# Kernel tuning notes

Hardware: AMD Instinct MI355X
Metric: run time of the kernel (lower is better)

Reference implementation:

```python
import math
import jax, jax.numpy as jnp
import numpy as np

B, S, D, H, V = 8, 1024, 512, 8, 32000
HD = D // H


def _position_embedding(seq_len, d_model):
    pos = jnp.arange(seq_len, dtype=jnp.float32)[:, None]                 # [S,1]
    div = jnp.exp(jnp.arange(0, d_model, 2, dtype=jnp.float32) * (-math.log(10000.0) / d_model))  # [D/2]
    ang = pos * div                                                        # [S,D/2]
    # interleave sin (even cols) / cos (odd cols)
    return jnp.stack([jnp.sin(ang), jnp.cos(ang)], axis=-1).reshape(seq_len, d_model)


def _min_max_normalize(w):
    lo = jnp.min(w, axis=-1, keepdims=True)
    hi = jnp.max(w, axis=-1, keepdims=True)
    return (w - lo) / (hi - lo)


def _converable_mask(h, Wc, bc):
    bs, seq = h.shape[0], h.shape[1]
    half = seq // 2
    shift = math.ceil(seq / 2)
    width = jnp.einsum('bsd,od->bso', h, Wc)[..., 0] + bc[0]               # [B,S]
    width = _min_max_normalize(width)[..., None]                           # [B,S,1]
    origin = jnp.concatenate([jnp.linspace(1.0, 0.0, half),
                              jnp.linspace(0.0, 1.0, seq - half)])         # [S]
    origin_mask = 1.0 - jax.nn.sigmoid((origin[None, None, :] - width) * 100.0)  # [B,S,S]
    idx = (jnp.arange(seq - 1, -1, -1)[:, None] + jnp.arange(seq)[None, :]) % seq  # [S,S]
    idx = jnp.roll(idx, shift, axis=0)
    # torch.roll of a [1,S] row along dim 0 is a no-op
    cmp = idx >= jnp.arange(seq)[None, :]                                  # [S,S] bool
    move = jnp.concatenate([cmp[:shift], ~cmp[shift:]], axis=0)            # [S,S]
    gathered = jnp.take_along_axis(origin_mask, idx[None, :, :], axis=2)   # [B,S,S]
    return gathered * move.astype(origin_mask.dtype)


def setup_inputs():
    key = jax.random.key(0)
    ks = jax.random.split(key, 9)
    s_emb = 1.0
    s_hd = 1.0 / math.sqrt(HD)
    s_d = 1.0 / math.sqrt(D)
    return {
        'x':   jax.random.randint(ks[0], (B, S), 0, V),
        'emb': jax.random.normal(ks[1], (V, D), dtype=jnp.float32) * s_emb,
        'Wq':  jax.random.normal(ks[2], (HD, HD), dtype=jnp.float32) * s_hd,
        'Wk':  jax.random.normal(ks[3], (HD, HD), dtype=jnp.float32) * s_hd,
        'Wv':  jax.random.normal(ks[4], (HD, HD), dtype=jnp.float32) * s_hd,
        'Wo':  jax.random.normal(ks[5], (D, D), dtype=jnp.float32) * s_d,
        'bo':  jnp.zeros((D,), dtype=jnp.float32),
        'Wc':  jax.random.normal(ks[6], (1, D), dtype=jnp.float32) * s_d,
        'bc':  jnp.zeros((1,), dtype=jnp.float32),
    }


def reference(x, emb, Wq, Wk, Wv, Wo, bo, Wc, bc):
    h = emb[x] + _position_embedding(S, D)[None]                           # [B,S,D]
    mask = _converable_mask(h, Wc, bc)                                     # [B,S,S]
    hh = h.reshape(B, S, H, HD)
    q = jnp.einsum('bshd,od->bsho', hh, Wq)
    k = jnp.einsum('bshd,od->bsho', hh, Wk)
    v = jnp.einsum('bshd,od->bsho', hh, Wv)
    energy = jnp.einsum('bqhd,bkhd->bhqk', q, k)                           # [B,H,S,S]
    # mask [B,S,S] broadcasts as [1,B,S,S]; valid because B == H (as in original)
    energy = energy * mask
    attn = jax.nn.softmax(energy / math.sqrt(D), axis=3)
    out = jnp.einsum('bhqk,bkhd->bqhd', attn, v).reshape(B, S, D)
    out = out @ Wo.T + bo
    return (out, mask)
```

## Files before the change

### kernel.cpp

```cpp
#include <hip/hip_runtime.h>
#include <hip/hip_bf16.h>
#include <math.h>

#define Bn 8
#define Sn 1024
#define Dn 512
#define Hn 8
#define HDn 64

typedef __bf16 bf16x8 __attribute__((ext_vector_type(8)));
typedef __bf16 bf16x4 __attribute__((ext_vector_type(4)));
typedef __bf16 bf16x2 __attribute__((ext_vector_type(2)));
typedef float  f32x4  __attribute__((ext_vector_type(4)));
typedef float  f32x16 __attribute__((ext_vector_type(16)));
typedef unsigned int u32x4 __attribute__((ext_vector_type(4)));

__device__ __forceinline__ unsigned enc_f(float v) {
    unsigned u = __float_as_uint(v);
    return (u & 0x80000000u) ? ~u : (u | 0x80000000u);
}
__device__ __forceinline__ float dec_f(unsigned k) {
    unsigned u = (k & 0x80000000u) ? (k ^ 0x80000000u) : ~k;
    return __uint_as_float(u);
}

__global__ __launch_bounds__(256) void k_fused(
        const int* __restrict__ x, const float* __restrict__ emb,
        const float* __restrict__ Wc, const float* __restrict__ bc,
        const float* __restrict__ Wq, const float* __restrict__ Wk,
        const float* __restrict__ Wv,
        float* __restrict__ width, unsigned* __restrict__ lohi,
        __bf16* __restrict__ q, __bf16* __restrict__ k, __bf16* __restrict__ vt) {
    __shared__ __align__(16) __bf16 Xs[64][72];
    __shared__ __align__(16) __bf16 WqS[64][72];
    __shared__ __align__(16) __bf16 WkS[64][72];
    __shared__ __align__(16) __bf16 WvS[64][72];
    __shared__ float wtok[8];
    int t = threadIdx.x;
    int bs0 = blockIdx.x * 8;
    int m0 = blockIdx.x * 64;
    int w = t >> 6, lane = t & 63, quad = lane >> 4, li = lane & 15;

    {
        int token = t >> 5, l32 = t & 31;
        int bs = bs0 + token;
        int s = bs & (Sn - 1);
        int tok = x[bs];
        float wpart = 0.f;
        int row = token * 8 + ((l32 * 16) >> 6);
        #pragma unroll
        for (int j = 0; j < 4; ++j) {
            int d0 = l32 * 16 + j * 4;
            float4 ev = *(const float4*)&emb[(size_t)tok * Dn + d0];
            float4 wc = *(const float4*)&Wc[d0];
            float hv[4];
            #pragma unroll
            for (int i = 0; i < 4; ++i) {
                int d = d0 + i;
                float f = __expf((float)(d & ~1) * (-9.210340371976184f / 512.0f));
                float ang = (float)s * f;
                float pe = (d & 1) ? __cosf(ang) : __sinf(ang);
                hv[i] = (&ev.x)[i] + pe;
                wpart += hv[i] * (&wc.x)[i];
            }
            *(bf16x4*)&Xs[row][d0 & 63] =
                (bf16x4){(__bf16)hv[0], (__bf16)hv[1], (__bf16)hv[2], (__bf16)hv[3]};
        }
        #pragma unroll
        for (int off = 1; off < 32; off <<= 1) wpart += __shfl_xor(wpart, off);
        if (l32 == 0) { float wv = wpart + bc[0]; width[bs] = wv; wtok[token] = wv; }
    }
    #pragma unroll
    for (int it = 0; it < 4; ++it) {
        int e = (it * 256 + t) * 4; int r = e >> 6, c = e & 63;
        float4 qv = *(const float4*)&Wq[e];
        *(bf16x4*)&WqS[r][c] = (bf16x4){(__bf16)qv.x, (__bf16)qv.y, (__bf16)qv.z, (__bf16)qv.w};
        float4 kv = *(const float4*)&Wk[e];
        *(bf16x4*)&WkS[r][c] = (bf16x4){(__bf16)kv.x, (__bf16)kv.y, (__bf16)kv.z, (__bf16)kv.w};
        float4 vv = *(const float4*)&Wv[e];
        *(bf16x4*)&WvS[r][c] = (bf16x4){(__bf16)vv.x, (__bf16)vv.y, (__bf16)vv.z, (__bf16)vv.w};
    }
    __syncthreads();

    if (t == 0) {
        float mn = wtok[0], mx = wtok[0];
        #pragma unroll
        for (int i = 1; i < 8; ++i) { mn = fminf(mn, wtok[i]); mx = fmaxf(mx, wtok[i]); }
        int b = bs0 >> 10;
        atomicMin(&lohi[b], enc_f(mn));
        atomicMin(&lohi[8 + b], ~enc_f(mx));
    }

    bf16x8 A0 = *(const bf16x8*)&Xs[w * 16 + li][quad * 8];
    bf16x8 A1 = *(const bf16x8*)&Xs[w * 16 + li][32 + quad * 8];
    f32x4 aq[4], ak[4], av[4];
    #pragma unroll
    for (int n = 0; n < 4; ++n) {
        aq[n] = (f32x4){0.f,0.f,0.f,0.f}; ak[n] = aq[n]; av[n] = aq[n];
        bf16x8 Bq0 = *(const bf16x8*)&WqS[n * 16 + li][quad * 8];
        bf16x8 Bq1 = *(const bf16x8*)&WqS[n * 16 + li][32 + quad * 8];
        aq[n] = __builtin_amdgcn_mfma_f32_16x16x32_bf16(A0, Bq0, aq[n], 0, 0, 0);
        aq[n] = __builtin_amdgcn_mfma_f32_16x16x32_bf16(A1, Bq1, aq[n], 0, 0, 0);
        bf16x8 Bk0 = *(const bf16x8*)&WkS[n * 16 + li][quad * 8];
        bf16x8 Bk1 = *(const bf16x8*)&WkS[n * 16 + li][32 + quad * 8];
        ak[n] = __builtin_amdgcn_mfma_f32_16x16x32_bf16(A0, Bk0, ak[n], 0, 0, 0);
        ak[n] = __builtin_amdgcn_mfma_f32_16x16x32_bf16(A1, Bk1, ak[n], 0, 0, 0);
        bf16x8 Bv0 = *(const bf16x8*)&WvS[n * 16 + li][quad * 8];
        bf16x8 Bv1 = *(const bf16x8*)&WvS[n * 16 + li][32 + quad * 8];
        av[n] = __builtin_amdgcn_mfma_f32_16x16x32_bf16(A0, Bv0, av[n], 0, 0, 0);
        av[n] = __builtin_amdgcn_mfma_f32_16x16x32_bf16(A1, Bv1, av[n], 0, 0, 0);
    }

    #pragma unroll
    for (int n = 0; n < 4; ++n)
        #pragma unroll
        for (int r = 0; r < 4; ++r) {
            int Rg = m0 + w * 16 + quad * 4 + r;
            int bsI = Rg >> 3, head = Rg & 7;
            int b = bsI >> 10, s = bsI & (Sn - 1);
            size_t oidx = (((size_t)(b * Hn + head)) * Sn + s) * HDn + n * 16 + li;
            q[oidx] = (__bf16)aq[n][r];
            k[oidx] = (__bf16)ak[n][r];
        }

    __bf16 (*Vs)[72] = WqS;
    __syncthreads();
    #pragma unroll
    for (int n = 0; n < 4; ++n)
        #pragma unroll
        for (int r = 0; r < 4; ++r)
            Vs[w * 16 + quad * 4 + r][n * 16 + li] = (__bf16)av[n][r];
    __syncthreads();
    int bs0i = m0 >> 3;
    int b = bs0i >> 10, s0l = bs0i & (Sn - 1);
    #pragma unroll
    for (int i = 0; i < 2; ++i) {
        int p = t + 256 * i;
        int head = p >> 6, o = p & 63;
        __bf16 tmp[8];
        #pragma unroll
        for (int j = 0; j < 8; ++j) tmp[j] = Vs[j * 8 + head][o];
        *(bf16x8*)&vt[(((size_t)(b * Hn + head)) * HDn + o) * Sn + s0l] = *(bf16x8*)tmp;
    }
}

__global__ void k_mask(const float* __restrict__ width, const unsigned* __restrict__ lohi,
                       float* __restrict__ mask_out, __bf16* __restrict__ maskb) {
    const float SCALE = 0.04419417382415922f;
    int bs = blockIdx.x;
    int b = bs >> 10;
    int s = bs & (Sn - 1);
    float lo = dec_f(lohi[b]);
    float hi = dec_f(~lohi[8 + b]);
    float wn = (width[bs] - lo) / (hi - lo);
    for (int t = threadIdx.x; t < Sn; t += 256) {
        int it = (t - s + 1535) & (Sn - 1);
        float origin = (it < 512) ? (1.0f - (float)it * (1.0f / 511.0f))
                                  : ((float)(it - 512) * (1.0f / 511.0f));
        float z = (origin - wn) * 100.0f;
        float om;
        if (z >= 0.0f) { float e = __expf(-z); om = e / (1.0f + e); }
        else           { float e = __expf(z);  om = 1.0f / (1.0f + e); }
        bool cmpv = (it >= t);
        bool mv = (s < 512) ? cmpv : !cmpv;
        float val = mv ? om : 0.0f;
        mask_out[(size_t)bs * Sn + t] = val;
        maskb[(size_t)bs * Sn + t] = (__bf16)(val * SCALE);
    }
}

__global__ __launch_bounds__(256, 2) void k_attn(
        const __bf16* __restrict__ q, const __bf16* __restrict__ k,
        const __bf16* __restrict__ vt, const __bf16* __restrict__ maskb,
        __bf16* __restrict__ ao) {
    __shared__ __align__(16) __bf16 Ks[2][64][72];
    __shared__ __align__(16) __bf16 Vt[2][64][72];
    int blk = blockIdx.x;
    int hh = blk & 7;
    int qt = (blk >> 3) & 7;
    int b  = blk >> 6;
    int bh = b * Hn + hh;
    int q0 = qt * 128;
    int t = threadIdx.x;
    int w = t >> 6, lane = t & 63, hi5 = lane >> 5, l31 = lane & 31;

    const __bf16* qbase  = q  + ((size_t)bh * Sn + q0 + w * 32) * HDn;
    const __bf16* kbase  = k  + (size_t)bh * Sn * HDn;
    const __bf16* vtbase = vt + (size_t)bh * HDn * Sn;
    const __bf16* mq = maskb + ((size_t)hh * Sn + q0 + w * 32 + l31) * Sn;

    bf16x8 Qf[4];
    #pragma unroll
    for (int c = 0; c < 4; ++c)
        Qf[c] = *(const bf16x8*)&qbase[(size_t)l31 * HDn + c * 16 + hi5 * 8];

    int sr0 = t >> 3, sc0 = (t & 7) * 8;
    bf16x8 pk0, pk1, pv0, pv1;
    pk0 = *(const bf16x8*)&kbase[(size_t)sr0 * HDn + sc0];
    pk1 = *(const bf16x8*)&kbase[(size_t)(sr0 + 32) * HDn + sc0];
    pv0 = *(const bf16x8*)&vtbase[(size_t)sr0 * Sn + sc0];
    pv1 = *(const bf16x8*)&vtbase[(size_t)(sr0 + 32) * Sn + sc0];
    *(bf16x8*)&Ks[0][sr0][sc0] = pk0;
    *(bf16x8*)&Ks[0][sr0 + 32][sc0] = pk1;
    *(bf16x8*)&Vt[0][sr0][sc0] = pv0;
    *(bf16x8*)&Vt[0][sr0 + 32][sc0] = pv1;
    __syncthreads();

    f32x16 OT[2];
    OT[0] = (f32x16){0.f,0.f,0.f,0.f,0.f,0.f,0.f,0.f,0.f,0.f,0.f,0.f,0.f,0.f,0.f,0.f};
    OT[1] = OT[0];
    float rs = 0.f;

    for (int ti = 0; ti < 16; ++ti) {
        int cur = ti & 1;

        bf16x4 mk[2][4];
        #pragma unroll
        for (int kg = 0; kg < 2; ++kg)
            #pragma unroll
            for (int g = 0; g < 4; ++g)
                mk[kg][g] = *(const bf16x4*)&mq[ti * 64 + kg * 32 + g * 8 + hi5 * 4];

        if (ti < 15) {
            int k0n = (ti + 1) * 64;
            pk0 = *(const bf16x8*)&kbase[(size_t)(k0n + sr0) * HDn + sc0];
            pk1 = *(const bf16x8*)&kbase[(size_t)(k0n + sr0 + 32) * HDn + sc0];
            pv0 = *(const bf16x8*)&vtbase[(size_t)sr0 * Sn + k0n + sc0];
            pv1 = *(const bf16x8*)&vtbase[(size_t)(sr0 + 32) * Sn + k0n + sc0];
        }

        f32x16 St[2];
        St[0] = (f32x16){0.f,0.f,0.f,0.f,0.f,0.f,0.f,0.f,0.f,0.f,0.f,0.f,0.f,0.f,0.f,0.f};
        St[1] = St[0];
        __builtin_amdgcn_s_setprio(1);
        #pragma unroll
        for (int c = 0; c < 4; ++c) {
            bf16x8 K0 = *(const bf16x8*)&Ks[cur][l31][c * 16 + hi5 * 8];
            St[0] = __builtin_amdgcn_mfma_f32_32x32x16_bf16(K0, Qf[c], St[0], 0, 0, 0);
            bf16x8 K1 = *(const bf16x8*)&Ks[cur][32 + l31][c * 16 + hi5 * 8];
            St[1] = __builtin_amdgcn_mfma_f32_32x32x16_bf16(K1, Qf[c], St[1], 0, 0, 0);
        }
        __builtin_amdgcn_s_setprio(0);

        unsigned pkd[2][4][2];
        #pragma unroll
        for (int kg = 0; kg < 2; ++kg) {
            #pragma unroll
            for (int g = 0; g < 4; ++g) {
                float p0 = __expf(St[kg][4 * g + 0] * (float)mk[kg][g][0]);
                float p1 = __expf(St[kg][4 * g + 1] * (float)mk[kg][g][1]);
                float p2 = __expf(St[kg][4 * g + 2] * (float)mk[kg][g][2]);
                float p3 = __expf(St[kg][4 * g + 3] * (float)mk[kg][g][3]);
                rs += (p0 + p1) + (p2 + p3);
                bf16x2 plo = { (__bf16)p0, (__bf16)p1 };
                bf16x2 phi = { (__bf16)p2, (__bf16)p3 };
                pkd[kg][g][0] = __builtin_bit_cast(unsigned, plo);
                pkd[kg][g][1] = __builtin_bit_cast(unsigned, phi);
            }
        }

        __builtin_amdgcn_s_setprio(1);
        #pragma unroll
        for (int c = 0; c < 4; ++c) {
            const int kg = c >> 1, gA = 2 * (c & 1), gB = gA + 1;
            unsigned z0 = hi5 ? pkd[kg][gB][0] : pkd[kg][gA][0];
            unsigned z1 = hi5 ? pkd[kg][gB][1] : pkd[kg][gA][1];
            unsigned y0 = hi5 ? pkd[kg][gA][0] : pkd[kg][gB][0];
            unsigned y1 = hi5 ? pkd[kg][gA][1] : pkd[kg][gB][1];
            unsigned x0 = (unsigned)__shfl_xor((int)y0, 32);
            unsigned x1 = (unsigned)__shfl_xor((int)y1, 32);
            u32x4 du;
            du[0] = hi5 ? x0 : z0;
            du[1] = hi5 ? x1 : z1;
            du[2] = hi5 ? z0 : x0;
            du[3] = hi5 ? z1 : x1;
            bf16x8 Pf = __builtin_bit_cast(bf16x8, du);
            bf16x8 V0 = *(const bf16x8*)&Vt[cur][l31][c * 16 + hi5 * 8];
            OT[0] = __builtin_amdgcn_mfma_f32_32x32x16_bf16(V0, Pf, OT[0], 0, 0, 0);
            bf16x8 V1 = *(const bf16x8*)&Vt[cur][32 + l31][c * 16 + hi5 * 8];
            OT[1] = __builtin_amdgcn_mfma_f32_32x32x16_bf16(V1, Pf, OT[1], 0, 0, 0);
        }
        __builtin_amdgcn_s_setprio(0);

        if (ti < 15) {
            *(bf16x8*)&Ks[cur ^ 1][sr0][sc0] = pk0;
            *(bf16x8*)&Ks[cur ^ 1][sr0 + 32][sc0] = pk1;
            *(bf16x8*)&Vt[cur ^ 1][sr0][sc0] = pv0;
            *(bf16x8*)&Vt[cur ^ 1][sr0 + 32][sc0] = pv1;
            __syncthreads();
        }
    }

    rs += __shfl_xor(rs, 32);
    float inv = __fdividef(1.0f, rs);

    size_t orow = ((size_t)b * Sn + q0 + w * 32 + l31) * Dn + hh * HDn;
    #pragma unroll
    for (int og = 0; og < 2; ++og)
        #pragma unroll
        for (int g2 = 0; g2 < 4; ++g2) {
            bf16x4 ov = { (__bf16)(OT[og][4 * g2 + 0] * inv),
                          (__bf16)(OT[og][4 * g2 + 1] * inv),
                          (__bf16)(OT[og][4 * g2 + 2] * inv),
                          (__bf16)(OT[og][4 * g2 + 3] * inv) };
            *(bf16x4*)&ao[orow + og * 32 + g2 * 8 + hi5 * 4] = ov;
        }
}

__global__ __launch_bounds__(256) void k_proj(
        const __bf16* __restrict__ ao, const float* __restrict__ Wo,
        const float* __restrict__ bo, float* __restrict__ out) {
    __shared__ __align__(16) __bf16 As[64][72];
    __shared__ __align__(16) __bf16 Bs[64][72];
    int bm = blockIdx.x >> 3;
    int bn = blockIdx.x & 7;
    int m0 = bm * 64, n0 = bn * 64;
    int t = threadIdx.x;
    int w = t >> 6, lane = t & 63, quad = lane >> 4, li = lane & 15;

    f32x4 O[4];
    #pragma unroll
    for (int n = 0; n < 4; ++n) O[n] = (f32x4){0.f, 0.f, 0.f, 0.f};

    for (int k0 = 0; k0 < Dn; k0 += 64) {
        if (k0) __syncthreads();
        #pragma unroll
        for (int it = 0; it < 2; ++it) {
            int e = (it * 256 + t) * 8; int r = e >> 6, c = e & 63;
            *(bf16x8*)&As[r][c] = *(const bf16x8*)&ao[(size_t)(m0 + r) * Dn + k0 + c];
        }
        #pragma unroll
        for (int it = 0; it < 4; ++it) {
            int e = (it * 256 + t) * 4; int r = e >> 6, c = e & 63;
            float4 wv = *(const float4*)&Wo[(size_t)(n0 + r) * Dn + k0 + c];
            *(bf16x4*)&Bs[r][c] = (bf16x4){(__bf16)wv.x, (__bf16)wv.y, (__bf16)wv.z, (__bf16)wv.w};
        }
        __syncthreads();

        bf16x8 A0 = *(const bf16x8*)&As[w * 16 + li][quad * 8];
        bf16x8 A1 = *(const bf16x8*)&As[w * 16 + li][32 + quad * 8];
        #pragma unroll
        for (int n = 0; n < 4; ++n) {
            bf16x8 B0 = *(const bf16x8*)&Bs[n * 16 + li][quad * 8];
            O[n] = __builtin_amdgcn_mfma_f32_16x16x32_bf16(A0, B0, O[n], 0, 0, 0);
            bf16x8 B1 = *(const bf16x8*)&Bs[n * 16 + li][32 + quad * 8];
            O[n] = __builtin_amdgcn_mfma_f32_16x16x32_bf16(A1, B1, O[n], 0, 0, 0);
        }
    }

    #pragma unroll
    for (int n = 0; n < 4; ++n) {
        float bias = bo[n0 + n * 16 + li];
        #pragma unroll
        for (int r = 0; r < 4; ++r)
            out[(size_t)(m0 + w * 16 + quad * 4 + r) * Dn + n0 + n * 16 + li] = O[n][r] + bias;
    }
}

extern "C" void kernel_launch(void* const* d_in, const int* in_sizes, int n_in,
                              void* d_out, int out_size, void* d_ws, size_t ws_size,
                              hipStream_t stream) {
    const int*   x   = (const int*)d_in[0];
    const float* emb = (const float*)d_in[1];
    const float* Wq  = (const float*)d_in[2];
    const float* Wk  = (const float*)d_in[3];
    const float* Wv  = (const float*)d_in[4];
    const float* Wo  = (const float*)d_in[5];
    const float* bo  = (const float*)d_in[6];
    const float* Wc  = (const float*)d_in[7];
    const float* bc  = (const float*)d_in[8];

    float* ws      = (float*)d_ws;
    float* width   = ws;
    unsigned* lohi = (unsigned*)(width + Bn * Sn);
    __bf16* qb   = (__bf16*)(ws + Bn * Sn + 16);
    __bf16* kb   = qb + (size_t)Bn * Sn * Dn;
    __bf16* vtb  = kb + (size_t)Bn * Sn * Dn;
    __bf16* maskb = vtb + (size_t)Bn * Sn * Dn;
    __bf16* ao   = maskb + (size_t)Bn * Sn * Sn;

    float* out      = (float*)d_out;
    float* mask_out = out + (size_t)Bn * Sn * Dn;

    hipMemsetAsync(lohi, 0xFF, 16 * sizeof(unsigned), stream);
    k_fused<<<(Bn * Sn) / 8, 256, 0, stream>>>(x, emb, Wc, bc, Wq, Wk, Wv,
                                               width, lohi, qb, kb, vtb);
    k_mask<<<Bn * Sn, 256, 0, stream>>>(width, lohi, mask_out, maskb);
    k_attn<<<Bn * Hn * (Sn / 128), 256, 0, stream>>>(qb, kb, vtb, maskb, ao);
    k_proj<<<(Bn * Sn / 64) * (Dn / 64), 256, 0, stream>>>(ao, Wo, bo, out);
}
```

Measured before the change: 208.1 us.

## Drop bf16 mask copy, fold scale into Q, shrink attention blocks, coalesce stores

The separate bf16 scaled mask buffer is removed. Attention now reads the fp32 mask output directly, and the softmax scale is folded into Q in the projection kernel. Q/K stores in the fused kernel and the output stores in the projection kernel are staged through shared memory so each thread writes contiguous vectors. The attention kernel moves to 128-thread blocks covering 64 query rows each, doubling the grid. The trade is half the mask traffic and better store coalescing against twice the fp32 mask bytes read per attention tile and extra syncs.

```diff
diff --git a/kernel.cpp b/kernel.cpp
--- a/kernel.cpp
+++ b/kernel.cpp
@@ -111,26 +111,32 @@
         av[n] = __builtin_amdgcn_mfma_f32_16x16x32_bf16(A1, Bv1, av[n], 0, 0, 0);
     }
 
+    const float SCALE = 0.04419417382415922f;
+    __syncthreads();
     #pragma unroll
     for (int n = 0; n < 4; ++n)
         #pragma unroll
         for (int r = 0; r < 4; ++r) {
-            int Rg = m0 + w * 16 + quad * 4 + r;
-            int bsI = Rg >> 3, head = Rg & 7;
-            int b = bsI >> 10, s = bsI & (Sn - 1);
-            size_t oidx = (((size_t)(b * Hn + head)) * Sn + s) * HDn + n * 16 + li;
-            q[oidx] = (__bf16)aq[n][r];
-            k[oidx] = (__bf16)ak[n][r];
-        }
+            int row = w * 16 + quad * 4 + r, col = n * 16 + li;
+            WkS[row][col] = (__bf16)(aq[n][r] * SCALE);
+            WvS[row][col] = (__bf16)ak[n][r];
+            WqS[row][col] = (__bf16)av[n][r];
+        }
+    __syncthreads();
+
+    {
+        int row = t >> 2, part = (t & 3) * 16;
+        int Rg = m0 + row;
+        int bsI = Rg >> 3, head = Rg & 7;
+        int bq = bsI >> 10, sq = bsI & (Sn - 1);
+        size_t base = (((size_t)(bq * Hn + head)) * Sn + sq) * HDn + part;
+        *(bf16x8*)&q[base]     = *(bf16x8*)&WkS[row][part];
+        *(bf16x8*)&q[base + 8] = *(bf16x8*)&WkS[row][part + 8];
+        *(bf16x8*)&k[base]     = *(bf16x8*)&WvS[row][part];
+        *(bf16x8*)&k[base + 8] = *(bf16x8*)&WvS[row][part + 8];
+    }
 
     __bf16 (*Vs)[72] = WqS;
-    __syncthreads();
-    #pragma unroll
-    for (int n = 0; n < 4; ++n)
-        #pragma unroll
-        for (int r = 0; r < 4; ++r)
-            Vs[w * 16 + quad * 4 + r][n * 16 + li] = (__bf16)av[n][r];
-    __syncthreads();
     int bs0i = m0 >> 3;
     int b = bs0i >> 10, s0l = bs0i & (Sn - 1);
     #pragma unroll
@@ -145,8 +151,7 @@
 }
 
 __global__ void k_mask(const float* __restrict__ width, const unsigned* __restrict__ lohi,
-                       float* __restrict__ mask_out, __bf16* __restrict__ maskb) {
-    const float SCALE = 0.04419417382415922f;
+                       float* __restrict__ mask_out) {
     int bs = blockIdx.x;
     int b = bs >> 10;
     int s = bs & (Sn - 1);
@@ -163,47 +168,47 @@
         else           { float e = __expf(z);  om = 1.0f / (1.0f + e); }
         bool cmpv = (it >= t);
         bool mv = (s < 512) ? cmpv : !cmpv;
-        float val = mv ? om : 0.0f;
-        mask_out[(size_t)bs * Sn + t] = val;
-        maskb[(size_t)bs * Sn + t] = (__bf16)(val * SCALE);
-    }
-}
-
-__global__ __launch_bounds__(256, 2) void k_attn(
+        mask_out[(size_t)bs * Sn + t] = mv ? om : 0.0f;
+    }
+}
+
+__global__ __launch_bounds__(128, 2) void k_attn(
         const __bf16* __restrict__ q, const __bf16* __restrict__ k,
-        const __bf16* __restrict__ vt, const __bf16* __restrict__ maskb,
+        const __bf16* __restrict__ vt, const float* __restrict__ mask,
         __bf16* __restrict__ ao) {
     __shared__ __align__(16) __bf16 Ks[2][64][72];
     __shared__ __align__(16) __bf16 Vt[2][64][72];
     int blk = blockIdx.x;
     int hh = blk & 7;
-    int qt = (blk >> 3) & 7;
-    int b  = blk >> 6;
+    int qt = (blk >> 3) & 15;
+    int b  = blk >> 7;
     int bh = b * Hn + hh;
-    int q0 = qt * 128;
+    int q0 = qt * 64;
     int t = threadIdx.x;
     int w = t >> 6, lane = t & 63, hi5 = lane >> 5, l31 = lane & 31;
 
     const __bf16* qbase  = q  + ((size_t)bh * Sn + q0 + w * 32) * HDn;
     const __bf16* kbase  = k  + (size_t)bh * Sn * HDn;
     const __bf16* vtbase = vt + (size_t)bh * HDn * Sn;
-    const __bf16* mq = maskb + ((size_t)hh * Sn + q0 + w * 32 + l31) * Sn;
+    const float* mq = mask + ((size_t)hh * Sn + q0 + w * 32 + l31) * Sn;
 
     bf16x8 Qf[4];
     #pragma unroll
     for (int c = 0; c < 4; ++c)
         Qf[c] = *(const bf16x8*)&qbase[(size_t)l31 * HDn + c * 16 + hi5 * 8];
 
-    int sr0 = t >> 3, sc0 = (t & 7) * 8;
-    bf16x8 pk0, pk1, pv0, pv1;
-    pk0 = *(const bf16x8*)&kbase[(size_t)sr0 * HDn + sc0];
-    pk1 = *(const bf16x8*)&kbase[(size_t)(sr0 + 32) * HDn + sc0];
-    pv0 = *(const bf16x8*)&vtbase[(size_t)sr0 * Sn + sc0];
-    pv1 = *(const bf16x8*)&vtbase[(size_t)(sr0 + 32) * Sn + sc0];
-    *(bf16x8*)&Ks[0][sr0][sc0] = pk0;
-    *(bf16x8*)&Ks[0][sr0 + 32][sc0] = pk1;
-    *(bf16x8*)&Vt[0][sr0][sc0] = pv0;
-    *(bf16x8*)&Vt[0][sr0 + 32][sc0] = pv1;
+    int sr = t >> 3, sc = (t & 7) * 8;
+    bf16x8 pk[4], pv[4];
+    #pragma unroll
+    for (int j = 0; j < 4; ++j) {
+        pk[j] = *(const bf16x8*)&kbase[(size_t)(sr + j * 16) * HDn + sc];
+        pv[j] = *(const bf16x8*)&vtbase[(size_t)(sr + j * 16) * Sn + sc];
+    }
+    #pragma unroll
+    for (int j = 0; j < 4; ++j) {
+        *(bf16x8*)&Ks[0][sr + j * 16][sc] = pk[j];
+        *(bf16x8*)&Vt[0][sr + j * 16][sc] = pv[j];
+    }
     __syncthreads();
 
     f32x16 OT[2];
@@ -214,19 +219,20 @@
     for (int ti = 0; ti < 16; ++ti) {
         int cur = ti & 1;
 
-        bf16x4 mk[2][4];
+        float4 mk[2][4];
         #pragma unroll
         for (int kg = 0; kg < 2; ++kg)
             #pragma unroll
             for (int g = 0; g < 4; ++g)
-                mk[kg][g] = *(const bf16x4*)&mq[ti * 64 + kg * 32 + g * 8 + hi5 * 4];
+                mk[kg][g] = *(const float4*)&mq[ti * 64 + kg * 32 + g * 8 + hi5 * 4];
 
         if (ti < 15) {
             int k0n = (ti + 1) * 64;
-            pk0 = *(const bf16x8*)&kbase[(size_t)(k0n + sr0) * HDn + sc0];
-            pk1 = *(const bf16x8*)&kbase[(size_t)(k0n + sr0 + 32) * HDn + sc0];
-            pv0 = *(const bf16x8*)&vtbase[(size_t)sr0 * Sn + k0n + sc0];
-            pv1 = *(const bf16x8*)&vtbase[(size_t)(sr0 + 32) * Sn + k0n + sc0];
+            #pragma unroll
+            for (int j = 0; j < 4; ++j) {
+                pk[j] = *(const bf16x8*)&kbase[(size_t)(k0n + sr + j * 16) * HDn + sc];
+                pv[j] = *(const bf16x8*)&vtbase[(size_t)(sr + j * 16) * Sn + k0n + sc];
+            }
         }
 
         f32x16 St[2];
@@ -247,10 +253,10 @@
         for (int kg = 0; kg < 2; ++kg) {
             #pragma unroll
             for (int g = 0; g < 4; ++g) {
-                float p0 = __expf(St[kg][4 * g + 0] * (float)mk[kg][g][0]);
-                float p1 = __expf(St[kg][4 * g + 1] * (float)mk[kg][g][1]);
-                float p2 = __expf(St[kg][4 * g + 2] * (float)mk[kg][g][2]);
-                float p3 = __expf(St[kg][4 * g + 3] * (float)mk[kg][g][3]);
+                float p0 = __expf(St[kg][4 * g + 0] * mk[kg][g].x);
+                float p1 = __expf(St[kg][4 * g + 1] * mk[kg][g].y);
+                float p2 = __expf(St[kg][4 * g + 2] * mk[kg][g].z);
+                float p3 = __expf(St[kg][4 * g + 3] * mk[kg][g].w);
                 rs += (p0 + p1) + (p2 + p3);
                 bf16x2 plo = { (__bf16)p0, (__bf16)p1 };
                 bf16x2 phi = { (__bf16)p2, (__bf16)p3 };
@@ -283,10 +289,11 @@
         __builtin_amdgcn_s_setprio(0);
 
         if (ti < 15) {
-            *(bf16x8*)&Ks[cur ^ 1][sr0][sc0] = pk0;
-            *(bf16x8*)&Ks[cur ^ 1][sr0 + 32][sc0] = pk1;
-            *(bf16x8*)&Vt[cur ^ 1][sr0][sc0] = pv0;
-            *(bf16x8*)&Vt[cur ^ 1][sr0 + 32][sc0] = pv1;
+            #pragma unroll
+            for (int j = 0; j < 4; ++j) {
+                *(bf16x8*)&Ks[cur ^ 1][sr + j * 16][sc] = pk[j];
+                *(bf16x8*)&Vt[cur ^ 1][sr + j * 16][sc] = pv[j];
+            }
             __syncthreads();
         }
     }
@@ -312,6 +319,7 @@
         const float* __restrict__ bo, float* __restrict__ out) {
     __shared__ __align__(16) __bf16 As[64][72];
     __shared__ __align__(16) __bf16 Bs[64][72];
+    __shared__ __align__(16) float  Os[64][68];
     int bm = blockIdx.x >> 3;
     int bn = blockIdx.x & 7;
     int m0 = bm * 64, n0 = bn * 64;
@@ -353,7 +361,15 @@
         float bias = bo[n0 + n * 16 + li];
         #pragma unroll
         for (int r = 0; r < 4; ++r)
-            out[(size_t)(m0 + w * 16 + quad * 4 + r) * Dn + n0 + n * 16 + li] = O[n][r] + bias;
+            Os[w * 16 + quad * 4 + r][n * 16 + li] = O[n][r] + bias;
+    }
+    __syncthreads();
+    {
+        int row = t >> 2, part = (t & 3) * 16;
+        size_t base = (size_t)(m0 + row) * Dn + n0 + part;
+        #pragma unroll
+        for (int j = 0; j < 4; ++j)
+            *(float4*)&out[base + j * 4] = *(const float4*)&Os[row][part + j * 4];
     }
 }
 
@@ -376,8 +392,7 @@
     __bf16* qb   = (__bf16*)(ws + Bn * Sn + 16);
     __bf16* kb   = qb + (size_t)Bn * Sn * Dn;
     __bf16* vtb  = kb + (size_t)Bn * Sn * Dn;
-    __bf16* maskb = vtb + (size_t)Bn * Sn * Dn;
-    __bf16* ao   = maskb + (size_t)Bn * Sn * Sn;
+    __bf16* ao   = vtb + (size_t)Bn * Sn * Dn;
 
     float* out      = (float*)d_out;
     float* mask_out = out + (size_t)Bn * Sn * Dn;
@@ -385,7 +400,7 @@
     hipMemsetAsync(lohi, 0xFF, 16 * sizeof(unsigned), stream);
     k_fused<<<(Bn * Sn) / 8, 256, 0, stream>>>(x, emb, Wc, bc, Wq, Wk, Wv,
                                                width, lohi, qb, kb, vtb);
-    k_mask<<<Bn * Sn, 256, 0, stream>>>(width, lohi, mask_out, maskb);
-    k_attn<<<Bn * Hn * (Sn / 128), 256, 0, stream>>>(qb, kb, vtb, maskb, ao);
+    k_mask<<<Bn * Sn, 256, 0, stream>>>(width, lohi, mask_out);
+    k_attn<<<Bn * Hn * (Sn / 64), 128, 0, stream>>>(qb, kb, vtb, mask_out, ao);
     k_proj<<<(Bn * Sn / 64) * (Dn / 64), 256, 0, stream>>>(ao, Wo, bo, out);
 }
```

After: 221.6 us. 1.06x slower.
